# Kernel tuning notes

Measured on AMD Instinct MI355X. Metric: run time of the kernel, lower is better.

The kernel has to match this reference:

```python
import jax, jax.numpy as jnp
import numpy as np

EPS = 1e-5

def causal_conv1d(x, w, b, groups=1):
    # x: [B,C,L], w: [O, C//groups, K]; left-pad K-1 => causal, length preserved
    k = w.shape[-1]
    x = jnp.pad(x, ((0, 0), (0, 0), (k - 1, 0)))
    y = jax.lax.conv_general_dilated(x, w, (1,), 'VALID',
        dimension_numbers=('NCH', 'OIH', 'NCH'), feature_group_count=groups)
    return y + b[None, :, None]

def bn_eval(x, g, b):
    # BatchNorm1d eval with init running stats (mean=0, var=1)
    scale = g / jnp.sqrt(1.0 + EPS)
    return x * scale[None, :, None] + b[None, :, None]

def maxpool1d(x, k):
    B, C, L = x.shape
    return x.reshape(B, C, L // k, k).max(-1)

def mamba2_layer(u, Wi, cw, cb, dt_bias, A_log, Dh, norm_w, Wo):
    Bb, L, _ = u.shape
    H = dt_bias.shape[0]
    d_inner = norm_w.shape[0]
    P = d_inner // H
    conv_dim = cw.shape[0]
    N = (conv_dim - d_inner) // 2
    zxbcdt = u @ Wi                                   # [B,L,2*d_inner+2N+H]
    z = zxbcdt[..., :d_inner]
    xBC = zxbcdt[..., d_inner:d_inner + conv_dim]
    dt = zxbcdt[..., d_inner + conv_dim:]
    xBC = causal_conv1d(xBC.swapaxes(1, 2), cw[:, None, :], cb, groups=conv_dim)
    xBC = jax.nn.silu(xBC).swapaxes(1, 2)             # [B,L,conv_dim]
    xs = xBC[..., :d_inner].reshape(Bb, L, H, P)
    Bm = xBC[..., d_inner:d_inner + N]                # [B,L,N] (ngroups=1)
    Cm = xBC[..., d_inner + N:]                       # [B,L,N]
    dt = jax.nn.softplus(dt + dt_bias)                # [B,L,H]
    dA = jnp.exp(dt * (-jnp.exp(A_log)))              # [B,L,H]
    dtx = dt[..., None] * xs                          # [B,L,H,P]
    def step(h, inp):
        dA_t, dtx_t, B_t, C_t = inp
        h = h * dA_t[:, :, None, None] + dtx_t[..., None] * B_t[:, None, None, :]
        y = jnp.einsum('bhpn,bn->bhp', h, C_t)
        return h, y
    h0 = jnp.zeros((Bb, H, P, N), u.dtype)
    _, ys = jax.lax.scan(step, h0, (dA.swapaxes(0, 1), dtx.swapaxes(0, 1),
                                    Bm.swapaxes(0, 1), Cm.swapaxes(0, 1)))
    y = ys.swapaxes(0, 1) + Dh[None, None, :, None] * xs
    y = y.reshape(Bb, L, d_inner)
    y = y * jax.nn.silu(z)                            # gate then RMSNorm (norm_before_gate=False)
    y = y * jax.lax.rsqrt(jnp.mean(y * y, axis=-1, keepdims=True) + EPS) * norm_w
    return y @ Wo

def forward(x, idx, patch_w, patch_b, conv_w, conv_b, bn_g, bn_b,
            cls_token, pos_embed, Wi, cw, cb, dt_bias, A_log, Dh,
            norm_w, Wo, ln_g, ln_b, fc_w, fc_b):
    # PatchEmbed: Conv2d kernel (patch_size,1) on [B,1,patch_size,L] -> [B,E,L]
    h = jnp.einsum('bpl,ep->bel', x[:, 0], patch_w) + patch_b[None, :, None]
    # CausalCNN (eval mode: dropout = identity)
    h = jax.nn.relu(bn_eval(causal_conv1d(h, conv_w[0], conv_b[0]), bn_g[0], bn_b[0]))
    h = jax.nn.relu(bn_eval(causal_conv1d(h, conv_w[1], conv_b[1]), bn_g[1], bn_b[1]))
    h = maxpool1d(h, 3)
    h = jax.nn.relu(bn_eval(causal_conv1d(h, conv_w[2], conv_b[2]), bn_g[2], bn_b[2]))
    h = jax.nn.relu(bn_eval(causal_conv1d(h, conv_w[3], conv_b[3]), bn_g[3], bn_b[3]))
    h = maxpool1d(h, 2)
    h = h.swapaxes(1, 2)                              # [B, num_patches, E]
    h = h + pos_embed[:, 1:, :]
    cls = cls_token + pos_embed[:, :1, :]
    h = jnp.concatenate([jnp.broadcast_to(cls, (h.shape[0], 1, h.shape[2])), h], axis=1)
    def block(carry, p):
        return carry + mamba2_layer(carry, *p), None
    h, _ = jax.lax.scan(block, h, (Wi, cw, cb, dt_bias, A_log, Dh, norm_w, Wo))
    mu = h.mean(-1, keepdims=True)
    var = ((h - mu) ** 2).mean(-1, keepdims=True)
    h = (h - mu) * jax.lax.rsqrt(var + EPS) * ln_g + ln_b
    h = h[:, 1:, :]                                   # drop cls
    agg = idx // 6                                    # aggregate_idx
    mask = (jnp.arange(h.shape[1])[None, :] <= agg[:, None]).astype(h.dtype)
    pooled = (h * mask[..., None]).sum(1) / (agg + 1).astype(h.dtype)[:, None]
    return pooled @ fc_w + fc_b

def _sincos_pos_embed(E, L):
    pos = np.arange(L, dtype=np.float32)
    omega = 1.0 / 10000 ** (np.arange(E // 2, dtype=np.float32) / (E / 2.0))
    out = pos[:, None] * omega[None, :]
    emb = np.concatenate([np.sin(out), np.cos(out)], axis=1)
    emb = np.concatenate([np.zeros((1, E), np.float32), emb], axis=0)  # cls row
    return jnp.asarray(emb)[None]

def setup_inputs() -> dict:
    key = jax.random.key(0)
    ks = jax.random.split(key, 12)
    B, E, Lm, Psz = 16, 256, 12288, 8
    depth, H, N, d_inner, K = 8, 8, 128, 512, 4
    conv_dim = d_inner + 2 * N        # 768
    dproj = 2 * d_inner + 2 * N + H   # 1288
    NC = 100
    NP = Lm // 6                      # 2048 patches
    f32 = jnp.float32
    dt0 = jax.random.uniform(ks[2], (depth, H), f32, 0.001, 0.1)
    return dict(
        x=jax.random.normal(ks[0], (B, 1, Psz, Lm), f32),
        idx=jax.random.randint(ks[1], (B,), 0, Lm),
        patch_w=jax.random.normal(ks[3], (E, Psz), f32) * 0.1,
        patch_b=jnp.zeros((E,), f32),
        conv_w=jax.random.normal(ks[4], (4, E, E, 5), f32) * 0.02,
        conv_b=jnp.zeros((4, E), f32),
        bn_g=jnp.ones((4, E), f32), bn_b=jnp.zeros((4, E), f32),
        cls_token=jax.random.normal(ks[5], (1, 1, E), f32) * 0.02,
        pos_embed=_sincos_pos_embed(E, NP),
        Wi=jax.random.normal(ks[6], (depth, E, dproj), f32) * 0.06,
        cw=jax.random.normal(ks[7], (depth, conv_dim, K), f32) * 0.2,
        cb=jnp.zeros((depth, conv_dim), f32),
        dt_bias=dt0 + jnp.log(-jnp.expm1(-dt0)),  # inverse softplus of dt
        A_log=jnp.log(jax.random.uniform(ks[8], (depth, H), f32, 1.0, 16.0)),
        Dh=jnp.ones((depth, H), f32),
        norm_w=jnp.ones((depth, d_inner), f32),
        Wo=jax.random.normal(ks[9], (depth, d_inner, E), f32) * 0.04,
        ln_g=jnp.ones((E,), f32), ln_b=jnp.zeros((E,), f32),
        fc_w=jax.random.normal(ks[10], (E, NC), f32) * 0.05,
        fc_b=jnp.zeros((NC,), f32),
    )

def reference(x, idx, patch_w, patch_b, conv_w, conv_b, bn_g, bn_b,
              cls_token, pos_embed, Wi, cw, cb, dt_bias, A_log, Dh,
              norm_w, Wo, ln_g, ln_b, fc_w, fc_b):
    return forward(x, idx, patch_w, patch_b, conv_w, conv_b, bn_g, bn_b,
                   cls_token, pos_embed, Wi, cw, cb, dt_bias, A_log, Dh,
                   norm_w, Wo, ln_g, ln_b, fc_w, fc_b)
```

## Files before the change

### kernel.cpp

```cpp
#include <hip/hip_runtime.h>
#include <cstdint>
#include <cstddef>

#define EPSF 1e-5f

typedef unsigned short u16;
typedef __attribute__((ext_vector_type(8))) short short8v;
typedef __attribute__((ext_vector_type(4))) float f32x4;

static __device__ __forceinline__ u16 f2bf(float f) {
  union { float f; unsigned u; } v; v.f = f;
  unsigned r = v.u + 0x7fffu + ((v.u >> 16) & 1u);
  return (u16)(r >> 16);
}
static __device__ __forceinline__ float bf2f(u16 h) {
  union { unsigned u; float f; } v; v.u = ((unsigned)h) << 16;
  return v.f;
}

__global__ void k_wconv(const float* __restrict__ src, u16* __restrict__ dst) {
  int i = blockIdx.x * 256 + threadIdx.x;
  if (i >= 4 * 256 * 256 * 5) return;
  int k = i % 5, r = i / 5;
  int ci = r & 255; r >>= 8;
  int co = r & 255; int l = r >> 8;
  dst[(((size_t)l * 256 + co) * 5 + k) * 256 + ci] = f2bf(src[i]);
}
__global__ void k_wti(const float* __restrict__ src, u16* __restrict__ dst) {
  int i = blockIdx.x * 256 + threadIdx.x;
  if (i >= 8 * 1288 * 256) return;
  int k = i & 255; int r = i >> 8;
  int n = r % 1288; int l = r / 1288;
  dst[i] = f2bf(src[((size_t)l * 256 + k) * 1288 + n]);
}
__global__ void k_wto(const float* __restrict__ src, u16* __restrict__ dst) {
  int i = blockIdx.x * 256 + threadIdx.x;
  if (i >= 8 * 256 * 512) return;
  int k = i & 511; int r = i >> 9;
  int n = r & 255; int l = r >> 8;
  dst[i] = f2bf(src[((size_t)l * 512 + k) * 256 + n]);
}

__global__ __launch_bounds__(256) void k_patchm(const float* __restrict__ x, const float* __restrict__ pw,
                                                const float* __restrict__ pb, u16* __restrict__ outb) {
  __shared__ float xs[8][64];
  const int l0 = blockIdx.x * 64;
  const int b = blockIdx.y;
  const int tid = threadIdx.x;
  const float* xb = x + (size_t)b * 8 * 12288;
  for (int q = tid; q < 512; q += 256) {
    int p = q >> 6, ll = q & 63;
    xs[p][ll] = xb[(size_t)p * 12288 + l0 + ll];
  }
  __syncthreads();
  float pwr[8];
#pragma unroll
  for (int p = 0; p < 8; ++p) pwr[p] = pw[tid * 8 + p];
  const float bias = pb[tid];
  u16* ob = outb + ((size_t)b * 12288 + l0) * 256 + tid;
  for (int ll = 0; ll < 64; ++ll) {
    float acc = bias;
#pragma unroll
    for (int p = 0; p < 8; ++p) acc += xs[p][ll] * pwr[p];
    ob[(size_t)ll * 256] = f2bf(acc);
  }
}

__global__ __launch_bounds__(256) void k_convm(const u16* __restrict__ in, const u16* __restrict__ wbf,
                                               const float* __restrict__ cbias, const float* __restrict__ bng,
                                               const float* __restrict__ bnb, u16* __restrict__ outb, int L) {
  __shared__ u16 Xs[132 * 40];
  __shared__ u16 Ws[64 * 168];
  const int l0 = blockIdx.x * 128;
  const int co0 = blockIdx.y * 64;
  const int b = blockIdx.z;
  const int tid = threadIdx.x;
  const int w = tid >> 6, l = tid & 63;
  const int mhalf = (w >> 1) * 64, nhalf = (w & 1) * 32;
  const u16* inb = in + (size_t)b * L * 256;
  u16* outbb = outb + (size_t)b * L * 256;
  f32x4 acc[4][2] = {};
  for (int ci0 = 0; ci0 < 256; ci0 += 32) {
    __syncthreads();
    for (int q = tid; q < 528; q += 256) {
      int row = q >> 2, coff = (q & 3) * 8;
      int gl = l0 - 4 + row;
      short8v v = {};
      if (gl >= 0) v = *(const short8v*)(inb + (size_t)gl * 256 + ci0 + coff);
      *(short8v*)(Xs + row * 40 + coff) = v;
    }
    for (int q = tid; q < 1280; q += 256) {
      int co = q / 20, rem = q % 20, k = rem >> 2, coff = (rem & 3) * 8;
      *(short8v*)(Ws + co * 168 + k * 32 + coff) =
          *(const short8v*)(wbf + ((size_t)(co0 + co) * 5 + k) * 256 + ci0 + coff);
    }
    __syncthreads();
    const int koff = (l >> 4) * 8;
    const int arow = mhalf + (l & 15);
    const int bro0 = (nhalf + (l & 15)) * 168;
    const int bro1 = (nhalf + 16 + (l & 15)) * 168;
#pragma unroll
    for (int k = 0; k < 5; ++k) {
      short8v b0 = *(const short8v*)(Ws + bro0 + k * 32 + koff);
      short8v b1 = *(const short8v*)(Ws + bro1 + k * 32 + koff);
#pragma unroll
      for (int mi = 0; mi < 4; ++mi) {
        short8v a = *(const short8v*)(Xs + (arow + mi * 16 + k) * 40 + koff);
        acc[mi][0] = __builtin_amdgcn_mfma_f32_16x16x32_bf16(a, b0, acc[mi][0], 0, 0, 0);
        acc[mi][1] = __builtin_amdgcn_mfma_f32_16x16x32_bf16(a, b1, acc[mi][1], 0, 0, 0);
      }
    }
  }
  const float scn = rsqrtf(1.f + EPSF);
#pragma unroll
  for (int ni = 0; ni < 2; ++ni) {
    int co = co0 + nhalf + ni * 16 + (l & 15);
    float alpha = bng[co] * scn;
    float beta = cbias[co] * alpha + bnb[co];
#pragma unroll
    for (int mi = 0; mi < 4; ++mi)
#pragma unroll
      for (int r = 0; r < 4; ++r) {
        int row = l0 + mhalf + mi * 16 + (l >> 4) * 4 + r;
        float v = acc[mi][ni][r] * alpha + beta;
        outbb[(size_t)row * 256 + co] = f2bf(fmaxf(v, 0.f));
      }
  }
}

__global__ void k_mpb(const u16* __restrict__ in, u16* __restrict__ out, int Lout, int kp, size_t total) {
  size_t i = (size_t)blockIdx.x * 256 + threadIdx.x;
  if (i >= total) return;
  size_t c = i & 255;
  size_t rest = i >> 8;
  size_t lo = rest % (size_t)Lout;
  size_t b = rest / (size_t)Lout;
  const u16* p = in + (b * (size_t)Lout * kp + lo * kp) * 256 + c;
  float m = bf2f(p[0]);
  for (int j = 1; j < kp; ++j) m = fmaxf(m, bf2f(p[(size_t)j * 256]));
  out[i] = f2bf(m);
}

__global__ __launch_bounds__(256) void k_asmb(const u16* __restrict__ in, const float* __restrict__ pos,
                                              const float* __restrict__ cls, float* __restrict__ uc,
                                              u16* __restrict__ ubc) {
  int t = blockIdx.x;
  int b = blockIdx.y;
  int e = threadIdx.x;
  float v;
  if (t == 0)
    v = cls[e] + pos[e];
  else
    v = bf2f(in[((size_t)b * 2048 + (t - 1)) * 256 + e]) + pos[(size_t)t * 256 + e];
  size_t o = ((size_t)b * 2049 + t) * 256 + e;
  uc[o] = v;
  ubc[o] = f2bf(v);
}

template <int MODE>
__global__ __launch_bounds__(256) void k_gemmm(const u16* __restrict__ A, const u16* __restrict__ BT,
                                               u16* __restrict__ OB, float* __restrict__ DT,
                                               float* __restrict__ C, u16* __restrict__ ubf,
                                               int M, int N, int K) {
  __shared__ u16 As[128 * 40];
  __shared__ u16 Bs[64 * 40];
  const int n0 = blockIdx.x * 64;
  const int m0 = blockIdx.y * 128;
  const int tid = threadIdx.x;
  const int w = tid >> 6, l = tid & 63;
  const int mhalf = (w >> 1) * 64, nhalf = (w & 1) * 32;
  f32x4 acc[4][2] = {};
  for (int k0 = 0; k0 < K; k0 += 32) {
    __syncthreads();
    for (int q = tid; q < 512; q += 256) {
      int row = q >> 2, koff = (q & 3) * 8;
      short8v v = {};
      if (m0 + row < M) v = *(const short8v*)(A + (size_t)(m0 + row) * K + k0 + koff);
      *(short8v*)(As + row * 40 + koff) = v;
    }
    {
      int row = tid >> 2, koff = (tid & 3) * 8;
      short8v v = {};
      if (n0 + row < N) v = *(const short8v*)(BT + (size_t)(n0 + row) * K + k0 + koff);
      *(short8v*)(Bs + row * 40 + koff) = v;
    }
    __syncthreads();
    const int koff = (l >> 4) * 8;
    short8v b0 = *(const short8v*)(Bs + (nhalf + (l & 15)) * 40 + koff);
    short8v b1 = *(const short8v*)(Bs + (nhalf + 16 + (l & 15)) * 40 + koff);
#pragma unroll
    for (int mi = 0; mi < 4; ++mi) {
      short8v a = *(const short8v*)(As + (mhalf + mi * 16 + (l & 15)) * 40 + koff);
      acc[mi][0] = __builtin_amdgcn_mfma_f32_16x16x32_bf16(a, b0, acc[mi][0], 0, 0, 0);
      acc[mi][1] = __builtin_amdgcn_mfma_f32_16x16x32_bf16(a, b1, acc[mi][1], 0, 0, 0);
    }
  }
#pragma unroll
  for (int mi = 0; mi < 4; ++mi)
#pragma unroll
    for (int r = 0; r < 4; ++r) {
      int m = m0 + mhalf + mi * 16 + (l >> 4) * 4 + r;
      if (m >= M) continue;
#pragma unroll
      for (int ni = 0; ni < 2; ++ni) {
        int n = n0 + nhalf + ni * 16 + (l & 15);
        if (n >= N) continue;
        float v = acc[mi][ni][r];
        if constexpr (MODE == 0) {
          if (n < 1280) OB[(size_t)m * 1280 + n] = f2bf(v);
          else DT[(size_t)m * 8 + (n - 1280)] = v;
        } else {
          float vv = C[(size_t)m * N + n] + v;
          C[(size_t)m * N + n] = vv;
          ubf[(size_t)m * N + n] = f2bf(vv);
        }
      }
    }
}

__global__ __launch_bounds__(256) void k_dw(const u16* __restrict__ zxb, const float* __restrict__ dtr,
                                            const float* __restrict__ cw, const float* __restrict__ cb,
                                            const float* __restrict__ dtbias, const float* __restrict__ al,
                                            u16* __restrict__ xBCb, float* __restrict__ dtb,
                                            float* __restrict__ ldb) {
  const int bx = blockIdx.x;
  const int t0 = blockIdx.y * 64;
  const int b = blockIdx.z;
  if (bx == 3) {
    int h = threadIdx.x & 7, ro = threadIdx.x >> 3;
    float dbv = dtbias[h];
    float av = expf(al[h]);
#pragma unroll
    for (int it = 0; it < 2; ++it) {
      int r = t0 + it * 32 + ro;
      if (r < 2049) {
        float v = dtr[((size_t)b * 2049 + r) * 8 + h] + dbv;
        float d = (v > 20.f) ? v : log1pf(expf(v));
        size_t o = ((size_t)b * 2049 + r) * 8 + h;
        dtb[o] = d;
        ldb[o] = -av * d;
      }
    }
    return;
  }
  int c = bx * 256 + threadIdx.x;
  const u16* col = zxb + ((size_t)b * 2049) * 1280 + 512 + c;
  float cw0 = cw[c * 4 + 0], cw1 = cw[c * 4 + 1], cw2 = cw[c * 4 + 2], cw3 = cw[c * 4 + 3];
  const float bias = cb[c];
  float w0 = 0.f, w1 = 0.f, w2 = 0.f;
  if (t0 - 3 >= 0) w0 = bf2f(col[(size_t)(t0 - 3) * 1280]);
  if (t0 - 2 >= 0) w1 = bf2f(col[(size_t)(t0 - 2) * 1280]);
  if (t0 - 1 >= 0) w2 = bf2f(col[(size_t)(t0 - 1) * 1280]);
  int tend = t0 + 64; if (tend > 2049) tend = 2049;
  u16* ob = xBCb + ((size_t)b * 2049) * 768 + c;
  for (int t = t0; t < tend; ++t) {
    float v = bf2f(col[(size_t)t * 1280]);
    float acc = bias + w0 * cw0 + w1 * cw1 + w2 * cw2 + v * cw3;
    float sig = 1.f / (1.f + expf(-acc));
    ob[(size_t)t * 768] = f2bf(acc * sig);
    w0 = w1; w1 = w2; w2 = v;
  }
}

__global__ __launch_bounds__(256) void k_ssd_intra(const u16* __restrict__ xBCb,
                                                   const float* __restrict__ dtg,
                                                   const float* __restrict__ ldg,
                                                   float* __restrict__ ybuf,
                                                   float* __restrict__ dtot) {
  const int L = 2049;
  const int c = blockIdx.x, h = blockIdx.y, b = blockIdx.z;
  const int tid = threadIdx.x;
  const int w = tid >> 6, l = tid & 63;
  const int t0 = c * 128;
  int qc = L - t0; if (qc > 128) qc = 128;

  __shared__ u16 R1[128 * 136];
  __shared__ u16 R2[128 * 136];
  __shared__ float dt_s[128], Lc_s[128];

  const u16* xb = xBCb + ((size_t)b * L) * 768;

  if (tid < 64) {
    int i2 = tid * 2;
    float a0 = 0.f, a1 = 0.f, d0 = 0.f, d1 = 0.f;
    if (i2 < qc) { size_t r = ((size_t)b * L + t0 + i2) * 8 + h; a0 = ldg[r]; d0 = dtg[r]; }
    if (i2 + 1 < qc) { size_t r = ((size_t)b * L + t0 + i2 + 1) * 8 + h; a1 = ldg[r]; d1 = dtg[r]; }
    dt_s[i2] = d0; dt_s[i2 + 1] = d1;
    float v = a0 + a1;
#pragma unroll
    for (int dlt = 1; dlt < 64; dlt <<= 1) {
      float t = __shfl_up(v, dlt, 64);
      if (tid >= dlt) v += t;
    }
    Lc_s[i2 + 1] = v;
    Lc_s[i2] = v - a1;
  }

  for (int q = tid; q < 2048; q += 256) {
    int row = q >> 4, off = (q & 15) * 8;
    short8v vb = {}, vc = {};
    if (row < qc) {
      const u16* src = xb + (size_t)(t0 + row) * 768;
      vb = *(const short8v*)(src + 512 + off);
      vc = *(const short8v*)(src + 640 + off);
    }
    *(short8v*)(R1 + row * 136 + off) = vb;
    *(short8v*)(R2 + row * 136 + off) = vc;
  }
  __syncthreads();

  const int wm = (w >> 1) * 64, wn = (w & 1) * 64;
  f32x4 g[4][4] = {};
  const bool skipG = (wm < wn);
  if (!skipG) {
#pragma unroll
    for (int ks = 0; ks < 4; ++ks) {
      const int koff = ks * 32 + (l >> 4) * 8;
      short8v bf[4];
#pragma unroll
      for (int ni = 0; ni < 4; ++ni)
        bf[ni] = *(const short8v*)(R1 + (wn + ni * 16 + (l & 15)) * 136 + koff);
#pragma unroll
      for (int mi = 0; mi < 4; ++mi) {
        short8v a = *(const short8v*)(R2 + (wm + mi * 16 + (l & 15)) * 136 + koff);
#pragma unroll
        for (int ni = 0; ni < 4; ++ni)
          g[mi][ni] = __builtin_amdgcn_mfma_f32_16x16x32_bf16(a, bf[ni], g[mi][ni], 0, 0, 0);
      }
    }
  }
  __syncthreads();

#pragma unroll
  for (int mi = 0; mi < 4; ++mi)
#pragma unroll
    for (int r = 0; r < 4; ++r) {
      int t = wm + mi * 16 + (l >> 4) * 4 + r;
      float lct = Lc_s[t];
#pragma unroll
      for (int ni = 0; ni < 4; ++ni) {
        int s = wn + ni * 16 + (l & 15);
        float v = 0.f;
        if (s <= t) v = __expf(lct - Lc_s[s]) * dt_s[s] * g[mi][ni][r];
        R2[t * 136 + s] = f2bf(v);
      }
    }
  for (int q = tid; q < 1024; q += 256) {
    int s = q >> 3, pv = (q & 7) * 8;
    short8v v = {};
    if (s < qc) v = *(const short8v*)(xb + (size_t)(t0 + s) * 768 + h * 64 + pv);
#pragma unroll
    for (int j = 0; j < 8; ++j) R1[(pv + j) * 136 + s] = (u16)v[j];
  }
  if (tid == 0) dtot[((size_t)b * 8 + h) * 17 + c] = __expf(Lc_s[qc - 1]);
  __syncthreads();

  {
    const int wmy = (w >> 1) * 64, wny = (w & 1) * 32;
    f32x4 ya[4][2] = {};
#pragma unroll
    for (int ks = 0; ks < 4; ++ks) {
      const int koff = ks * 32 + (l >> 4) * 8;
      short8v b0 = *(const short8v*)(R1 + (wny + (l & 15)) * 136 + koff);
      short8v b1 = *(const short8v*)(R1 + (wny + 16 + (l & 15)) * 136 + koff);
#pragma unroll
      for (int mi = 0; mi < 4; ++mi) {
        short8v a = *(const short8v*)(R2 + (wmy + mi * 16 + (l & 15)) * 136 + koff);
        ya[mi][0] = __builtin_amdgcn_mfma_f32_16x16x32_bf16(a, b0, ya[mi][0], 0, 0, 0);
        ya[mi][1] = __builtin_amdgcn_mfma_f32_16x16x32_bf16(a, b1, ya[mi][1], 0, 0, 0);
      }
    }
    float* yb = ybuf + ((size_t)b * L + t0) * 512 + h * 64;
#pragma unroll
    for (int mi = 0; mi < 4; ++mi)
#pragma unroll
      for (int r = 0; r < 4; ++r) {
        int t = wmy + mi * 16 + (l >> 4) * 4 + r;
        if (t >= qc) continue;
#pragma unroll
        for (int ni = 0; ni < 2; ++ni) {
          int p = wny + ni * 16 + (l & 15);
          yb[(size_t)t * 512 + p] = ya[mi][ni][r];
        }
      }
  }
}

__global__ __launch_bounds__(256) void k_ssd_state(const u16* __restrict__ xBCb,
                                                   const float* __restrict__ dtg,
                                                   const float* __restrict__ ldg,
                                                   float* __restrict__ sc) {
  const int L = 2049;
  const int c = blockIdx.x, h = blockIdx.y, b = blockIdx.z;
  const int tid = threadIdx.x;
  const int w = tid >> 6, l = tid & 63;
  const int t0 = c * 128;
  int qc = L - t0; if (qc > 128) qc = 128;

  __shared__ u16 XW[64 * 136];
  __shared__ u16 BT[128 * 136];
  __shared__ float dt_s[128], Lc_s[128];

  const u16* xb = xBCb + ((size_t)b * L) * 768;

  if (tid < 64) {
    int i2 = tid * 2;
    float a0 = 0.f, a1 = 0.f, d0 = 0.f, d1 = 0.f;
    if (i2 < qc) { size_t r = ((size_t)b * L + t0 + i2) * 8 + h; a0 = ldg[r]; d0 = dtg[r]; }
    if (i2 + 1 < qc) { size_t r = ((size_t)b * L + t0 + i2 + 1) * 8 + h; a1 = ldg[r]; d1 = dtg[r]; }
    dt_s[i2] = d0; dt_s[i2 + 1] = d1;
    float v = a0 + a1;
#pragma unroll
    for (int dlt = 1; dlt < 64; dlt <<= 1) {
      float t = __shfl_up(v, dlt, 64);
      if (tid >= dlt) v += t;
    }
    Lc_s[i2 + 1] = v;
    Lc_s[i2] = v - a1;
  }
  __syncthreads();

  const float Lend = Lc_s[qc - 1];
  for (int q = tid; q < 1024; q += 256) {
    int s = q >> 3, pv = (q & 7) * 8;
    float w2 = __expf(Lend - Lc_s[s]) * dt_s[s];
    short8v v = {};
    if (s < qc) v = *(const short8v*)(xb + (size_t)(t0 + s) * 768 + h * 64 + pv);
#pragma unroll
    for (int j = 0; j < 8; ++j) XW[(pv + j) * 136 + s] = f2bf(bf2f((u16)v[j]) * w2);
  }
  for (int q = tid; q < 2048; q += 256) {
    int s = q >> 4, nv = (q & 15) * 8;
    short8v v = {};
    if (s < qc) v = *(const short8v*)(xb + (size_t)(t0 + s) * 768 + 512 + nv);
#pragma unroll
    for (int j = 0; j < 8; ++j) BT[(nv + j) * 136 + s] = (u16)v[j];
  }
  __syncthreads();

  const int wms = (w & 1) * 32, wns = (w >> 1) * 64;
  f32x4 sa[2][4] = {};
#pragma unroll
  for (int ks = 0; ks < 4; ++ks) {
    const int koff = ks * 32 + (l >> 4) * 8;
    short8v a0 = *(const short8v*)(XW + (wms + (l & 15)) * 136 + koff);
    short8v a1 = *(const short8v*)(XW + (wms + 16 + (l & 15)) * 136 + koff);
#pragma unroll
    for (int ni = 0; ni < 4; ++ni) {
      short8v bb = *(const short8v*)(BT + (wns + ni * 16 + (l & 15)) * 136 + koff);
      sa[0][ni] = __builtin_amdgcn_mfma_f32_16x16x32_bf16(a0, bb, sa[0][ni], 0, 0, 0);
      sa[1][ni] = __builtin_amdgcn_mfma_f32_16x16x32_bf16(a1, bb, sa[1][ni], 0, 0, 0);
    }
  }
  float* scp = sc + (((size_t)b * 8 + h) * 17 + c) * 8192;
#pragma unroll
  for (int mi = 0; mi < 2; ++mi)
#pragma unroll
    for (int r = 0; r < 4; ++r) {
      int p = wms + mi * 16 + (l >> 4) * 4 + r;
#pragma unroll
      for (int ni = 0; ni < 4; ++ni) {
        int n = wns + ni * 16 + (l & 15);
        scp[p * 128 + n] = sa[mi][ni][r];
      }
    }
}

__global__ __launch_bounds__(256) void k_ssd_scan(float* __restrict__ sc, const float* __restrict__ dtot,
                                                  int nbh) {
  int gid = blockIdx.x * 256 + threadIdx.x;
  int bh = gid >> 13;
  if (bh >= nbh) return;
  int elem = gid & 8191;
  float* base = sc + (size_t)bh * 17 * 8192 + elem;
  const float* dtp = dtot + (size_t)bh * 17;
  float hc = 0.f;
#pragma unroll
  for (int cc = 0; cc < 17; ++cc) {
    float D = dtp[cc];
    float v = base[(size_t)cc * 8192];
    base[(size_t)cc * 8192] = hc;
    hc = hc * D + v;
  }
}

__global__ __launch_bounds__(256) void k_ssd_inter(const u16* __restrict__ xBCb,
                                                   const float* __restrict__ ldg,
                                                   const float* __restrict__ sc,
                                                   const float* __restrict__ Dh,
                                                   float* __restrict__ ybuf) {
  const int L = 2049;
  const int c = blockIdx.x, h = blockIdx.y, b = blockIdx.z;
  const int tid = threadIdx.x;
  const int w = tid >> 6, l = tid & 63;
  const int t0 = c * 128;
  int qc = L - t0; if (qc > 128) qc = 128;

  __shared__ u16 Cs[128 * 136];
  __shared__ u16 H0[64 * 136];
  __shared__ float Lc_s[128];

  const u16* xb = xBCb + ((size_t)b * L) * 768;

  if (tid < 64) {
    int i2 = tid * 2;
    float a0 = 0.f, a1 = 0.f;
    if (i2 < qc) a0 = ldg[((size_t)b * L + t0 + i2) * 8 + h];
    if (i2 + 1 < qc) a1 = ldg[((size_t)b * L + t0 + i2 + 1) * 8 + h];
    float v = a0 + a1;
#pragma unroll
    for (int dlt = 1; dlt < 64; dlt <<= 1) {
      float t = __shfl_up(v, dlt, 64);
      if (tid >= dlt) v += t;
    }
    Lc_s[i2 + 1] = v;
    Lc_s[i2] = v - a1;
  }
  for (int q = tid; q < 2048; q += 256) {
    int row = q >> 4, off = (q & 15) * 8;
    short8v vc = {};
    if (row < qc) vc = *(const short8v*)(xb + (size_t)(t0 + row) * 768 + 640 + off);
    *(short8v*)(Cs + row * 136 + off) = vc;
  }
  {
    const float* hp = sc + (((size_t)b * 8 + h) * 17 + c) * 8192;
    for (int q = tid; q < 8192; q += 256) {
      int p = q >> 7, n = q & 127;
      H0[p * 136 + n] = f2bf(hp[p * 128 + n]);
    }
  }
  __syncthreads();

  const int wm = (w >> 1) * 64, wn = (w & 1) * 32;
  f32x4 acc[4][2] = {};
#pragma unroll
  for (int ks = 0; ks < 4; ++ks) {
    const int koff = ks * 32 + (l >> 4) * 8;
    short8v b0 = *(const short8v*)(H0 + (wn + (l & 15)) * 136 + koff);
    short8v b1 = *(const short8v*)(H0 + (wn + 16 + (l & 15)) * 136 + koff);
#pragma unroll
    for (int mi = 0; mi < 4; ++mi) {
      short8v a = *(const short8v*)(Cs + (wm + mi * 16 + (l & 15)) * 136 + koff);
      acc[mi][0] = __builtin_amdgcn_mfma_f32_16x16x32_bf16(a, b0, acc[mi][0], 0, 0, 0);
      acc[mi][1] = __builtin_amdgcn_mfma_f32_16x16x32_bf16(a, b1, acc[mi][1], 0, 0, 0);
    }
  }
  const float DD = Dh[h];
  float* yb = ybuf + ((size_t)b * L + t0) * 512 + h * 64;
#pragma unroll
  for (int mi = 0; mi < 4; ++mi)
#pragma unroll
    for (int r = 0; r < 4; ++r) {
      int t = wm + mi * 16 + (l >> 4) * 4 + r;
      if (t >= qc) continue;
      float e = __expf(Lc_s[t]);
#pragma unroll
      for (int ni = 0; ni < 2; ++ni) {
        int p = wn + ni * 16 + (l & 15);
        float xs = bf2f(xb[(size_t)(t0 + t) * 768 + h * 64 + p]);
        yb[(size_t)t * 512 + p] += e * acc[mi][ni][r] + DD * xs;
      }
    }
}

__global__ __launch_bounds__(256) void k_gaterms(const float* __restrict__ y, const u16* __restrict__ zxb,
                                                 const float* __restrict__ nw, u16* __restrict__ y2,
                                                 int Mc) {
  int row = blockIdx.x * 4 + (threadIdx.x >> 6);
  if (row >= Mc) return;
  int lane = threadIdx.x & 63;
  const float* yr = y + (size_t)row * 512 + lane * 8;
  const u16* zr = zxb + (size_t)row * 1280 + lane * 8;
  short8v zv8 = *(const short8v*)zr;
  float g[8];
  float ss = 0.f;
#pragma unroll
  for (int j = 0; j < 8; ++j) {
    float yv = yr[j];
    float zv = bf2f((u16)zv8[j]);
    float sig = 1.f / (1.f + expf(-zv));
    float gg = yv * zv * sig;
    g[j] = gg;
    ss += gg * gg;
  }
#pragma unroll
  for (int off = 32; off > 0; off >>= 1) ss += __shfl_xor(ss, off);
  float r = rsqrtf(ss * (1.f / 512.f) + EPSF);
#pragma unroll
  for (int j = 0; j < 8; ++j)
    y2[(size_t)row * 512 + lane * 8 + j] = f2bf(g[j] * r * nw[lane * 8 + j]);
}

__global__ __launch_bounds__(256) void k_ln(const float* __restrict__ u, const float* __restrict__ g,
                                            const float* __restrict__ bb, float* __restrict__ out) {
  int rid = blockIdx.x * 4 + (threadIdx.x >> 6);
  int lane = threadIdx.x & 63;
  int b = rid >> 11;
  int t = (rid & 2047) + 1;
  const float* ur = u + ((size_t)b * 2049 + t) * 256 + lane * 4;
  float v[4];
  float s1 = 0.f, s2 = 0.f;
#pragma unroll
  for (int j = 0; j < 4; ++j) {
    v[j] = ur[j];
    s1 += v[j];
    s2 += v[j] * v[j];
  }
#pragma unroll
  for (int off = 32; off > 0; off >>= 1) {
    s1 += __shfl_xor(s1, off);
    s2 += __shfl_xor(s2, off);
  }
  float mu = s1 * (1.f / 256.f);
  float var = s2 * (1.f / 256.f) - mu * mu;
  float rs = rsqrtf(var + EPSF);
  float* orow = out + ((size_t)b * 2048 + (t - 1)) * 256 + lane * 4;
#pragma unroll
  for (int j = 0; j < 4; ++j) orow[j] = (v[j] - mu) * rs * g[lane * 4 + j] + bb[lane * 4 + j];
}

__global__ __launch_bounds__(256) void k_pp(const float* __restrict__ hln, const int* __restrict__ idx,
                                            float* __restrict__ part) {
  int ch = blockIdx.x;
  int b = blockIdx.y;
  int e = threadIdx.x;
  int agg = idx[b] / 6;
  int t0 = ch * 256;
  int tend = agg + 1 - t0;
  if (tend > 256) tend = 256;
  float s = 0.f;
  for (int i = 0; i < tend; ++i) s += hln[((size_t)b * 2048 + t0 + i) * 256 + e];
  part[((size_t)b * 8 + ch) * 256 + e] = s;
}

__global__ __launch_bounds__(256) void k_fc(const float* __restrict__ part, const int* __restrict__ idx,
                                            const float* __restrict__ fw, const float* __restrict__ fb,
                                            float* __restrict__ out) {
  __shared__ float pooled[256];
  int b = blockIdx.x;
  int tid = threadIdx.x;
  float s = 0.f;
#pragma unroll
  for (int ch = 0; ch < 8; ++ch) s += part[((size_t)b * 8 + ch) * 256 + tid];
  pooled[tid] = s;
  __syncthreads();
  if (tid < 100) {
    int agg = idx[b] / 6;
    float inv = 1.f / (float)(agg + 1);
    float acc = 0.f;
    for (int e = 0; e < 256; ++e) acc += pooled[e] * fw[e * 100 + tid];
    out[b * 100 + tid] = acc * inv + fb[tid];
  }
}

extern "C" void kernel_launch(void* const* d_in, const int* in_sizes, int n_in,
                              void* d_out, int out_size, void* d_ws, size_t ws_size,
                              hipStream_t stream) {
  (void)in_sizes; (void)n_in; (void)out_size;
  const float* x        = (const float*)d_in[0];
  const int*   idx      = (const int*)d_in[1];
  const float* patch_w  = (const float*)d_in[2];
  const float* patch_b  = (const float*)d_in[3];
  const float* conv_w   = (const float*)d_in[4];
  const float* conv_b   = (const float*)d_in[5];
  const float* bn_g     = (const float*)d_in[6];
  const float* bn_b     = (const float*)d_in[7];
  const float* cls_tok  = (const float*)d_in[8];
  const float* pos_emb  = (const float*)d_in[9];
  const float* Wi       = (const float*)d_in[10];
  const float* cw       = (const float*)d_in[11];
  const float* cb       = (const float*)d_in[12];
  const float* dt_bias  = (const float*)d_in[13];
  const float* A_log    = (const float*)d_in[14];
  const float* Dh       = (const float*)d_in[15];
  const float* norm_w   = (const float*)d_in[16];
  const float* Wo       = (const float*)d_in[17];
  const float* ln_g     = (const float*)d_in[18];
  const float* ln_b     = (const float*)d_in[19];
  const float* fc_w     = (const float*)d_in[20];
  const float* fc_b     = (const float*)d_in[21];
  float* out = (float*)d_out;
  float* ws = (float*)d_ws;

  auto need = [](size_t cb) {
    size_t Rsz = cb * 4835096ull;
    if (Rsz < 8388608ull) Rsz = 8388608ull;
    return (8392704ull + Rsz + 4096 + 1318912 + 524288 + 655360 + 32768 + cb * 262272ull) * 4ull;
  };
  size_t CB = 16;
  while (CB > 1 && ws_size < need(CB)) CB >>= 1;
  const int NCHUNK = (int)(16 / CB);
  const int Mc = (int)(CB * 2049);

  size_t Rsz = CB * 4835096ull;
  if (Rsz < 8388608ull) Rsz = 8388608ull;

  float* u   = ws;
  float* R   = u + 8392704;
  u16*  zxb  = (u16*)R;
  float* dtr = R + CB * 1311360;
  float* dtb = dtr + CB * 16392;
  float* ldb = dtb + CB * 16392;
  float* afterldb = ldb + CB * 16392;
  u16*  xBCb = (u16*)afterldb;
  float* ybuf = afterldb + CB * 786816;
  u16*  y2bf = (u16*)(ybuf + CB * 1049088);
  float* scb = ybuf + CB * 1049088 + CB * 524544;
  u16* fA = (u16*)R;
  u16* fB = (u16*)(R + CB * 1572864);
  float* hln = R;
  float* dtot = R + Rsz;
  u16*  WiT  = (u16*)(dtot + 4096);
  u16*  WoT  = (u16*)((float*)WiT + 1318912);
  u16*  wbf  = (u16*)((float*)WoT + 524288);
  float* ppar = (float*)wbf + 655360;
  u16*  u_bf = (u16*)(ppar + 32768);

  k_wconv<<<dim3((4 * 256 * 256 * 5 + 255) / 256), 256, 0, stream>>>(conv_w, wbf);
  k_wti<<<dim3((8 * 1288 * 256 + 255) / 256), 256, 0, stream>>>(Wi, WiT);
  k_wto<<<dim3((8 * 256 * 512 + 255) / 256), 256, 0, stream>>>(Wo, WoT);

  const unsigned gy = (unsigned)((Mc + 127) / 128);

  for (int bc = 0; bc < NCHUNK; ++bc) {
    const float* xc = x + (size_t)bc * CB * 8 * 12288;
    float* uc = u + (size_t)bc * CB * 2049 * 256;

    k_patchm<<<dim3(192, (unsigned)CB), 256, 0, stream>>>(xc, patch_w, patch_b, fA);
    k_convm<<<dim3(96, 4, (unsigned)CB), 256, 0, stream>>>(fA, wbf + 0 * 327680, conv_b + 0, bn_g + 0, bn_b + 0, fB, 12288);
    k_convm<<<dim3(96, 4, (unsigned)CB), 256, 0, stream>>>(fB, wbf + 1 * 327680, conv_b + 256, bn_g + 256, bn_b + 256, fA, 12288);
    {
      size_t tot = CB * 4096 * 256;
      k_mpb<<<dim3((unsigned)((tot + 255) / 256)), 256, 0, stream>>>(fA, fB, 4096, 3, tot);
    }
    k_convm<<<dim3(32, 4, (unsigned)CB), 256, 0, stream>>>(fB, wbf + 2 * 327680, conv_b + 512, bn_g + 512, bn_b + 512, fA, 4096);
    k_convm<<<dim3(32, 4, (unsigned)CB), 256, 0, stream>>>(fA, wbf + 3 * 327680, conv_b + 768, bn_g + 768, bn_b + 768, fB, 4096);
    {
      size_t tot = CB * 2048 * 256;
      k_mpb<<<dim3((unsigned)((tot + 255) / 256)), 256, 0, stream>>>(fB, fA, 2048, 2, tot);
    }
    k_asmb<<<dim3(2049, (unsigned)CB), 256, 0, stream>>>(fA, pos_emb, cls_tok, uc, u_bf);

    for (int l = 0; l < 8; ++l) {
      const u16* WiTl = WiT + (size_t)l * 1288 * 256;
      const u16* WoTl = WoT + (size_t)l * 256 * 512;
      const float* cwl  = cw + (size_t)l * 768 * 4;
      const float* cbl  = cb + (size_t)l * 768;
      const float* dtbl = dt_bias + l * 8;
      const float* all  = A_log + l * 8;
      const float* dhl  = Dh + l * 8;
      const float* nwl  = norm_w + (size_t)l * 512;

      k_gemmm<0><<<dim3(21, gy), 256, 0, stream>>>(u_bf, WiTl, zxb, dtr, nullptr, nullptr, Mc, 1288, 256);
      k_dw<<<dim3(4, 33, (unsigned)CB), 256, 0, stream>>>(zxb, dtr, cwl, cbl, dtbl, all, xBCb, dtb, ldb);
      k_ssd_intra<<<dim3(17, 8, (unsigned)CB), 256, 0, stream>>>(xBCb, dtb, ldb, ybuf, dtot);
      k_ssd_state<<<dim3(17, 8, (unsigned)CB), 256, 0, stream>>>(xBCb, dtb, ldb, scb);
      k_ssd_scan<<<dim3((unsigned)(CB * 8 * 32)), 256, 0, stream>>>(scb, dtot, (int)(CB * 8));
      k_ssd_inter<<<dim3(17, 8, (unsigned)CB), 256, 0, stream>>>(xBCb, ldb, scb, dhl, ybuf);
      k_gaterms<<<dim3((unsigned)((Mc + 3) / 4)), 256, 0, stream>>>(ybuf, zxb, nwl, y2bf, Mc);
      k_gemmm<1><<<dim3(4, gy), 256, 0, stream>>>(y2bf, WoTl, nullptr, nullptr, uc, u_bf, Mc, 256, 512);
    }
  }

  k_ln<<<dim3(8192), 256, 0, stream>>>(u, ln_g, ln_b, hln);
  k_pp<<<dim3(8, 16), 256, 0, stream>>>(hln, idx, ppar);
  k_fc<<<dim3(16), 256, 0, stream>>>(ppar, idx, fc_w, fc_b, out);
}
```

Baseline: 4.146 ms.

## Fold head dimension into SSD chunk kernels to reuse shared C·Bᵀ gram

The intra-chunk, state and inter-chunk SSD kernels now launch one block per (chunk, batch) and loop over all 8 heads inside the block. Head-independent work is done once per block: the C·Bᵀ gram matrix in the intra kernel and the B and C tile loads in the state and inter kernels. Each block also computes the per-head cumulative decay for all heads up front. In exchange the grid is 8x smaller and each block runs serially over heads with extra barriers, which may leave compute units idle when the batch is small.

```diff
diff --git a/kernel.cpp b/kernel.cpp
--- a/kernel.cpp
+++ b/kernel.cpp
@@ -268,7 +268,7 @@
                                                    float* __restrict__ ybuf,
                                                    float* __restrict__ dtot) {
   const int L = 2049;
-  const int c = blockIdx.x, h = blockIdx.y, b = blockIdx.z;
+  const int c = blockIdx.x, b = blockIdx.y;
   const int tid = threadIdx.x;
   const int w = tid >> 6, l = tid & 63;
   const int t0 = c * 128;
@@ -276,24 +276,29 @@
 
   __shared__ u16 R1[128 * 136];
   __shared__ u16 R2[128 * 136];
-  __shared__ float dt_s[128], Lc_s[128];
+  __shared__ float dt_all[8][128], Lc_all[8][128];
 
   const u16* xb = xBCb + ((size_t)b * L) * 768;
 
-  if (tid < 64) {
-    int i2 = tid * 2;
+  for (int hh = w; hh < 8; hh += 4) {
+    int i2 = l * 2;
     float a0 = 0.f, a1 = 0.f, d0 = 0.f, d1 = 0.f;
-    if (i2 < qc) { size_t r = ((size_t)b * L + t0 + i2) * 8 + h; a0 = ldg[r]; d0 = dtg[r]; }
-    if (i2 + 1 < qc) { size_t r = ((size_t)b * L + t0 + i2 + 1) * 8 + h; a1 = ldg[r]; d1 = dtg[r]; }
-    dt_s[i2] = d0; dt_s[i2 + 1] = d1;
+    if (i2 < qc) { size_t r = ((size_t)b * L + t0 + i2) * 8 + hh; a0 = ldg[r]; d0 = dtg[r]; }
+    if (i2 + 1 < qc) { size_t r = ((size_t)b * L + t0 + i2 + 1) * 8 + hh; a1 = ldg[r]; d1 = dtg[r]; }
+    dt_all[hh][i2] = d0; dt_all[hh][i2 + 1] = d1;
     float v = a0 + a1;
 #pragma unroll
     for (int dlt = 1; dlt < 64; dlt <<= 1) {
       float t = __shfl_up(v, dlt, 64);
-      if (tid >= dlt) v += t;
-    }
-    Lc_s[i2 + 1] = v;
-    Lc_s[i2] = v - a1;
+      if (l >= dlt) v += t;
+    }
+    Lc_all[hh][i2 + 1] = v;
+    Lc_all[hh][i2] = v - a1;
+    int lastlane = (qc - 1) >> 1;
+    if (l == lastlane) {
+      float lcend = ((qc - 1) & 1) ? v : (v - a1);
+      dtot[((size_t)b * 8 + hh) * 17 + c] = __expf(lcend);
+    }
   }
 
   for (int q = tid; q < 2048; q += 256) {
@@ -311,8 +316,7 @@
 
   const int wm = (w >> 1) * 64, wn = (w & 1) * 64;
   f32x4 g[4][4] = {};
-  const bool skipG = (wm < wn);
-  if (!skipG) {
+  if (wm >= wn) {
 #pragma unroll
     for (int ks = 0; ks < 4; ++ks) {
       const int koff = ks * 32 + (l >> 4) * 8;
@@ -331,31 +335,30 @@
   }
   __syncthreads();
 
-#pragma unroll
-  for (int mi = 0; mi < 4; ++mi)
-#pragma unroll
-    for (int r = 0; r < 4; ++r) {
-      int t = wm + mi * 16 + (l >> 4) * 4 + r;
-      float lct = Lc_s[t];
-#pragma unroll
-      for (int ni = 0; ni < 4; ++ni) {
-        int s = wn + ni * 16 + (l & 15);
-        float v = 0.f;
-        if (s <= t) v = __expf(lct - Lc_s[s]) * dt_s[s] * g[mi][ni][r];
-        R2[t * 136 + s] = f2bf(v);
-      }
-    }
-  for (int q = tid; q < 1024; q += 256) {
-    int s = q >> 3, pv = (q & 7) * 8;
-    short8v v = {};
-    if (s < qc) v = *(const short8v*)(xb + (size_t)(t0 + s) * 768 + h * 64 + pv);
-#pragma unroll
-    for (int j = 0; j < 8; ++j) R1[(pv + j) * 136 + s] = (u16)v[j];
-  }
-  if (tid == 0) dtot[((size_t)b * 8 + h) * 17 + c] = __expf(Lc_s[qc - 1]);
-  __syncthreads();
-
-  {
+  for (int h = 0; h < 8; ++h) {
+#pragma unroll
+    for (int mi = 0; mi < 4; ++mi)
+#pragma unroll
+      for (int r = 0; r < 4; ++r) {
+        int t = wm + mi * 16 + (l >> 4) * 4 + r;
+        float lct = Lc_all[h][t];
+#pragma unroll
+        for (int ni = 0; ni < 4; ++ni) {
+          int s = wn + ni * 16 + (l & 15);
+          float v = 0.f;
+          if (s <= t) v = __expf(lct - Lc_all[h][s]) * dt_all[h][s] * g[mi][ni][r];
+          R2[t * 136 + s] = f2bf(v);
+        }
+      }
+    for (int q = tid; q < 1024; q += 256) {
+      int s = q >> 3, pv = (q & 7) * 8;
+      short8v v = {};
+      if (s < qc) v = *(const short8v*)(xb + (size_t)(t0 + s) * 768 + h * 64 + pv);
+#pragma unroll
+      for (int j = 0; j < 8; ++j) R1[(pv + j) * 136 + s] = (u16)v[j];
+    }
+    __syncthreads();
+
     const int wmy = (w >> 1) * 64, wny = (w & 1) * 32;
     f32x4 ya[4][2] = {};
 #pragma unroll
@@ -383,6 +386,7 @@
           yb[(size_t)t * 512 + p] = ya[mi][ni][r];
         }
       }
+    __syncthreads();
   }
 }
 
@@ -391,44 +395,34 @@
                                                    const float* __restrict__ ldg,
                                                    float* __restrict__ sc) {
   const int L = 2049;
-  const int c = blockIdx.x, h = blockIdx.y, b = blockIdx.z;
+  const int c = blockIdx.x, b = blockIdx.y;
   const int tid = threadIdx.x;
   const int w = tid >> 6, l = tid & 63;
   const int t0 = c * 128;
   int qc = L - t0; if (qc > 128) qc = 128;
 
+  __shared__ u16 BT[128 * 136];
   __shared__ u16 XW[64 * 136];
-  __shared__ u16 BT[128 * 136];
-  __shared__ float dt_s[128], Lc_s[128];
+  __shared__ float dt_all[8][128], Lc_all[8][128];
 
   const u16* xb = xBCb + ((size_t)b * L) * 768;
 
-  if (tid < 64) {
-    int i2 = tid * 2;
+  for (int hh = w; hh < 8; hh += 4) {
+    int i2 = l * 2;
     float a0 = 0.f, a1 = 0.f, d0 = 0.f, d1 = 0.f;
-    if (i2 < qc) { size_t r = ((size_t)b * L + t0 + i2) * 8 + h; a0 = ldg[r]; d0 = dtg[r]; }
-    if (i2 + 1 < qc) { size_t r = ((size_t)b * L + t0 + i2 + 1) * 8 + h; a1 = ldg[r]; d1 = dtg[r]; }
-    dt_s[i2] = d0; dt_s[i2 + 1] = d1;
+    if (i2 < qc) { size_t r = ((size_t)b * L + t0 + i2) * 8 + hh; a0 = ldg[r]; d0 = dtg[r]; }
+    if (i2 + 1 < qc) { size_t r = ((size_t)b * L + t0 + i2 + 1) * 8 + hh; a1 = ldg[r]; d1 = dtg[r]; }
+    dt_all[hh][i2] = d0; dt_all[hh][i2 + 1] = d1;
     float v = a0 + a1;
 #pragma unroll
     for (int dlt = 1; dlt < 64; dlt <<= 1) {
       float t = __shfl_up(v, dlt, 64);
-      if (tid >= dlt) v += t;
-    }
-    Lc_s[i2 + 1] = v;
-    Lc_s[i2] = v - a1;
-  }
-  __syncthreads();
-
-  const float Lend = Lc_s[qc - 1];
-  for (int q = tid; q < 1024; q += 256) {
-    int s = q >> 3, pv = (q & 7) * 8;
-    float w2 = __expf(Lend - Lc_s[s]) * dt_s[s];
-    short8v v = {};
-    if (s < qc) v = *(const short8v*)(xb + (size_t)(t0 + s) * 768 + h * 64 + pv);
-#pragma unroll
-    for (int j = 0; j < 8; ++j) XW[(pv + j) * 136 + s] = f2bf(bf2f((u16)v[j]) * w2);
-  }
+      if (l >= dlt) v += t;
+    }
+    Lc_all[hh][i2 + 1] = v;
+    Lc_all[hh][i2] = v - a1;
+  }
+
   for (int q = tid; q < 2048; q += 256) {
     int s = q >> 4, nv = (q & 15) * 8;
     short8v v = {};
@@ -438,32 +432,46 @@
   }
   __syncthreads();
 
-  const int wms = (w & 1) * 32, wns = (w >> 1) * 64;
-  f32x4 sa[2][4] = {};
-#pragma unroll
-  for (int ks = 0; ks < 4; ++ks) {
-    const int koff = ks * 32 + (l >> 4) * 8;
-    short8v a0 = *(const short8v*)(XW + (wms + (l & 15)) * 136 + koff);
-    short8v a1 = *(const short8v*)(XW + (wms + 16 + (l & 15)) * 136 + koff);
-#pragma unroll
-    for (int ni = 0; ni < 4; ++ni) {
-      short8v bb = *(const short8v*)(BT + (wns + ni * 16 + (l & 15)) * 136 + koff);
-      sa[0][ni] = __builtin_amdgcn_mfma_f32_16x16x32_bf16(a0, bb, sa[0][ni], 0, 0, 0);
-      sa[1][ni] = __builtin_amdgcn_mfma_f32_16x16x32_bf16(a1, bb, sa[1][ni], 0, 0, 0);
-    }
-  }
-  float* scp = sc + (((size_t)b * 8 + h) * 17 + c) * 8192;
-#pragma unroll
-  for (int mi = 0; mi < 2; ++mi)
-#pragma unroll
-    for (int r = 0; r < 4; ++r) {
-      int p = wms + mi * 16 + (l >> 4) * 4 + r;
+  for (int h = 0; h < 8; ++h) {
+    const float Lend = Lc_all[h][qc - 1];
+    for (int q = tid; q < 1024; q += 256) {
+      int s = q >> 3, pv = (q & 7) * 8;
+      float w2 = __expf(Lend - Lc_all[h][s]) * dt_all[h][s];
+      short8v v = {};
+      if (s < qc) v = *(const short8v*)(xb + (size_t)(t0 + s) * 768 + h * 64 + pv);
+#pragma unroll
+      for (int j = 0; j < 8; ++j) XW[(pv + j) * 136 + s] = f2bf(bf2f((u16)v[j]) * w2);
+    }
+    __syncthreads();
+
+    const int wms = (w & 1) * 32, wns = (w >> 1) * 64;
+    f32x4 sa[2][4] = {};
+#pragma unroll
+    for (int ks = 0; ks < 4; ++ks) {
+      const int koff = ks * 32 + (l >> 4) * 8;
+      short8v a0 = *(const short8v*)(XW + (wms + (l & 15)) * 136 + koff);
+      short8v a1 = *(const short8v*)(XW + (wms + 16 + (l & 15)) * 136 + koff);
 #pragma unroll
       for (int ni = 0; ni < 4; ++ni) {
-        int n = wns + ni * 16 + (l & 15);
-        scp[p * 128 + n] = sa[mi][ni][r];
-      }
-    }
+        short8v bb = *(const short8v*)(BT + (wns + ni * 16 + (l & 15)) * 136 + koff);
+        sa[0][ni] = __builtin_amdgcn_mfma_f32_16x16x32_bf16(a0, bb, sa[0][ni], 0, 0, 0);
+        sa[1][ni] = __builtin_amdgcn_mfma_f32_16x16x32_bf16(a1, bb, sa[1][ni], 0, 0, 0);
+      }
+    }
+    float* scp = sc + (((size_t)b * 8 + h) * 17 + c) * 8192;
+#pragma unroll
+    for (int mi = 0; mi < 2; ++mi)
+#pragma unroll
+      for (int r = 0; r < 4; ++r) {
+        int p = wms + mi * 16 + (l >> 4) * 4 + r;
+#pragma unroll
+        for (int ni = 0; ni < 4; ++ni) {
+          int n = wns + ni * 16 + (l & 15);
+          scp[p * 128 + n] = sa[mi][ni][r];
+        }
+      }
+    __syncthreads();
+  }
 }
 
 __global__ __launch_bounds__(256) void k_ssd_scan(float* __restrict__ sc, const float* __restrict__ dtot,
@@ -490,7 +498,7 @@
                                                    const float* __restrict__ Dh,
                                                    float* __restrict__ ybuf) {
   const int L = 2049;
-  const int c = blockIdx.x, h = blockIdx.y, b = blockIdx.z;
+  const int c = blockIdx.x, b = blockIdx.y;
   const int tid = threadIdx.x;
   const int w = tid >> 6, l = tid & 63;
   const int t0 = c * 128;
@@ -498,69 +506,75 @@
 
   __shared__ u16 Cs[128 * 136];
   __shared__ u16 H0[64 * 136];
-  __shared__ float Lc_s[128];
+  __shared__ float Lc_all[8][128];
 
   const u16* xb = xBCb + ((size_t)b * L) * 768;
 
-  if (tid < 64) {
-    int i2 = tid * 2;
+  for (int hh = w; hh < 8; hh += 4) {
+    int i2 = l * 2;
     float a0 = 0.f, a1 = 0.f;
-    if (i2 < qc) a0 = ldg[((size_t)b * L + t0 + i2) * 8 + h];
-    if (i2 + 1 < qc) a1 = ldg[((size_t)b * L + t0 + i2 + 1) * 8 + h];
+    if (i2 < qc) a0 = ldg[((size_t)b * L + t0 + i2) * 8 + hh];
+    if (i2 + 1 < qc) a1 = ldg[((size_t)b * L + t0 + i2 + 1) * 8 + hh];
     float v = a0 + a1;
 #pragma unroll
     for (int dlt = 1; dlt < 64; dlt <<= 1) {
       float t = __shfl_up(v, dlt, 64);
-      if (tid >= dlt) v += t;
-    }
-    Lc_s[i2 + 1] = v;
-    Lc_s[i2] = v - a1;
-  }
+      if (l >= dlt) v += t;
+    }
+    Lc_all[hh][i2 + 1] = v;
+    Lc_all[hh][i2] = v - a1;
+  }
+
   for (int q = tid; q < 2048; q += 256) {
     int row = q >> 4, off = (q & 15) * 8;
     short8v vc = {};
     if (row < qc) vc = *(const short8v*)(xb + (size_t)(t0 + row) * 768 + 640 + off);
     *(short8v*)(Cs + row * 136 + off) = vc;
   }
-  {
-    const float* hp = sc + (((size_t)b * 8 + h) * 17 + c) * 8192;
-    for (int q = tid; q < 8192; q += 256) {
-      int p = q >> 7, n = q & 127;
-      H0[p * 136 + n] = f2bf(hp[p * 128 + n]);
-    }
-  }
   __syncthreads();
 
-  const int wm = (w >> 1) * 64, wn = (w & 1) * 32;
-  f32x4 acc[4][2] = {};
-#pragma unroll
-  for (int ks = 0; ks < 4; ++ks) {
-    const int koff = ks * 32 + (l >> 4) * 8;
-    short8v b0 = *(const short8v*)(H0 + (wn + (l & 15)) * 136 + koff);
-    short8v b1 = *(const short8v*)(H0 + (wn + 16 + (l & 15)) * 136 + koff);
-#pragma unroll
-    for (int mi = 0; mi < 4; ++mi) {
-      short8v a = *(const short8v*)(Cs + (wm + mi * 16 + (l & 15)) * 136 + koff);
-      acc[mi][0] = __builtin_amdgcn_mfma_f32_16x16x32_bf16(a, b0, acc[mi][0], 0, 0, 0);
-      acc[mi][1] = __builtin_amdgcn_mfma_f32_16x16x32_bf16(a, b1, acc[mi][1], 0, 0, 0);
-    }
-  }
-  const float DD = Dh[h];
-  float* yb = ybuf + ((size_t)b * L + t0) * 512 + h * 64;
-#pragma unroll
-  for (int mi = 0; mi < 4; ++mi)
-#pragma unroll
-    for (int r = 0; r < 4; ++r) {
-      int t = wm + mi * 16 + (l >> 4) * 4 + r;
-      if (t >= qc) continue;
-      float e = __expf(Lc_s[t]);
-#pragma unroll
-      for (int ni = 0; ni < 2; ++ni) {
-        int p = wn + ni * 16 + (l & 15);
-        float xs = bf2f(xb[(size_t)(t0 + t) * 768 + h * 64 + p]);
-        yb[(size_t)t * 512 + p] += e * acc[mi][ni][r] + DD * xs;
-      }
-    }
+  for (int h = 0; h < 8; ++h) {
+    {
+      const float* hp = sc + (((size_t)b * 8 + h) * 17 + c) * 8192;
+      for (int q = tid; q < 8192; q += 256) {
+        int p = q >> 7, n = q & 127;
+        H0[p * 136 + n] = f2bf(hp[p * 128 + n]);
+      }
+    }
+    __syncthreads();
+
+    const int wm = (w >> 1) * 64, wn = (w & 1) * 32;
+    f32x4 acc[4][2] = {};
+#pragma unroll
+    for (int ks = 0; ks < 4; ++ks) {
+      const int koff = ks * 32 + (l >> 4) * 8;
+      short8v b0 = *(const short8v*)(H0 + (wn + (l & 15)) * 136 + koff);
+      short8v b1 = *(const short8v*)(H0 + (wn + 16 + (l & 15)) * 136 + koff);
+#pragma unroll
+      for (int mi = 0; mi < 4; ++mi) {
+        short8v a = *(const short8v*)(Cs + (wm + mi * 16 + (l & 15)) * 136 + koff);
+        acc[mi][0] = __builtin_amdgcn_mfma_f32_16x16x32_bf16(a, b0, acc[mi][0], 0, 0, 0);
+        acc[mi][1] = __builtin_amdgcn_mfma_f32_16x16x32_bf16(a, b1, acc[mi][1], 0, 0, 0);
+      }
+    }
+    const float DD = Dh[h];
+    float* yb = ybuf + ((size_t)b * L + t0) * 512 + h * 64;
+#pragma unroll
+    for (int mi = 0; mi < 4; ++mi)
+#pragma unroll
+      for (int r = 0; r < 4; ++r) {
+        int t = wm + mi * 16 + (l >> 4) * 4 + r;
+        if (t >= qc) continue;
+        float e = __expf(Lc_all[h][t]);
+#pragma unroll
+        for (int ni = 0; ni < 2; ++ni) {
+          int p = wn + ni * 16 + (l & 15);
+          float xs = bf2f(xb[(size_t)(t0 + t) * 768 + h * 64 + p]);
+          yb[(size_t)t * 512 + p] += e * acc[mi][ni][r] + DD * xs;
+        }
+      }
+    __syncthreads();
+  }
 }
 
 __global__ __launch_bounds__(256) void k_gaterms(const float* __restrict__ y, const u16* __restrict__ zxb,
@@ -753,10 +767,10 @@
 
       k_gemmm<0><<<dim3(21, gy), 256, 0, stream>>>(u_bf, WiTl, zxb, dtr, nullptr, nullptr, Mc, 1288, 256);
       k_dw<<<dim3(4, 33, (unsigned)CB), 256, 0, stream>>>(zxb, dtr, cwl, cbl, dtbl, all, xBCb, dtb, ldb);
-      k_ssd_intra<<<dim3(17, 8, (unsigned)CB), 256, 0, stream>>>(xBCb, dtb, ldb, ybuf, dtot);
-      k_ssd_state<<<dim3(17, 8, (unsigned)CB), 256, 0, stream>>>(xBCb, dtb, ldb, scb);
+      k_ssd_intra<<<dim3(17, (unsigned)CB), 256, 0, stream>>>(xBCb, dtb, ldb, ybuf, dtot);
+      k_ssd_state<<<dim3(17, (unsigned)CB), 256, 0, stream>>>(xBCb, dtb, ldb, scb);
       k_ssd_scan<<<dim3((unsigned)(CB * 8 * 32)), 256, 0, stream>>>(scb, dtot, (int)(CB * 8));
-      k_ssd_inter<<<dim3(17, 8, (unsigned)CB), 256, 0, stream>>>(xBCb, ldb, scb, dhl, ybuf);
+      k_ssd_inter<<<dim3(17, (unsigned)CB), 256, 0, stream>>>(xBCb, ldb, scb, dhl, ybuf);
       k_gaterms<<<dim3((unsigned)((Mc + 3) / 4)), 256, 0, stream>>>(ybuf, zxb, nwl, y2bf, Mc);
       k_gemmm<1><<<dim3(4, gy), 256, 0, stream>>>(y2bf, WoTl, nullptr, nullptr, uc, u_bf, Mc, 256, 512);
     }
```

Measured after the change: 5.116 ms. 1.23x slower.
